# Kernel tuning notes

Hardware: AMD Instinct MI355X
Metric: run time of the kernel (lower is better)

Reference implementation:

```python
import jax, jax.numpy as jnp
import numpy as np

N = 50000      # nodes
E = 800000     # edges (avg degree 16)
F_IN = 128
HID = 128
C = 40
EPS = 1e-5     # BatchNorm1d eps


def setup_inputs() -> dict:
    key = jax.random.key(0)
    ks = jax.random.split(key, 8)

    def glorot(k, shape):
        lim = np.sqrt(6.0 / (shape[0] + shape[1])).astype(np.float32)
        return jax.random.uniform(k, shape, jnp.float32, -lim, lim)

    inp = {
        "features": jax.random.normal(ks[0], (N, F_IN), jnp.float32),
        "edge_index": jax.random.randint(ks[1], (2, E), 0, N, jnp.int32),
        "W1": glorot(ks[2], (F_IN, HID)), "b1": jnp.zeros((HID,), jnp.float32),
        "gamma1": jnp.ones((HID,), jnp.float32), "beta1": jnp.zeros((HID,), jnp.float32),
        "W2": glorot(ks[3], (HID, HID)), "b2": jnp.zeros((HID,), jnp.float32),
        "gamma2": jnp.ones((HID,), jnp.float32), "beta2": jnp.zeros((HID,), jnp.float32),
        "W3": glorot(ks[4], (HID, C)), "b3": jnp.zeros((C,), jnp.float32),
    }
    return inp


def _gcn_norm(edge_index):
    # Add self-loops and compute symmetric normalization D^-1/2 (A+I) D^-1/2
    loops = jnp.arange(N, dtype=edge_index.dtype)
    src = jnp.concatenate([edge_index[0], loops])
    dst = jnp.concatenate([edge_index[1], loops])
    deg = jax.ops.segment_sum(jnp.ones((E + N,), jnp.float32), dst, num_segments=N)
    dinv = jax.lax.rsqrt(jnp.maximum(deg, 1.0))
    return src, dst, dinv[src] * dinv[dst]  # per-edge norm coefficient


def _gcn_conv(x, W, b, src, dst, norm):
    h = x @ W                                   # [N, out]
    msg = h[src] * norm[:, None]                # gather + scale, [E+N, out]
    return jax.ops.segment_sum(msg, dst, num_segments=N) + b


def _bn(x, gamma, beta):
    # training-mode BatchNorm1d over the node axis (biased variance)
    mu = jnp.mean(x, axis=0)
    var = jnp.mean(jnp.square(x - mu), axis=0)
    return (x - mu) * jax.lax.rsqrt(var + EPS) * gamma + beta


def reference(features, edge_index, W1, b1, gamma1, beta1, W2, b2, gamma2, beta2, W3, b3):
    src, dst, norm = _gcn_norm(edge_index)
    h = jax.nn.relu(_bn(_gcn_conv(features, W1, b1, src, dst, norm), gamma1, beta1))
    h = jax.nn.relu(_bn(_gcn_conv(h, W2, b2, src, dst, norm), gamma2, beta2))
    h = _gcn_conv(h, W3, b3, src, dst, norm)
    return jax.nn.log_softmax(h, axis=-1)
```

## Files before the change

kernel.cpp:

```cpp
#include <hip/hip_runtime.h>
#include <math.h>

#define FEAT 128
#define NCLS 40
#define BN_EPS 1e-5f

typedef unsigned short u16;
typedef unsigned int u32;
typedef __attribute__((ext_vector_type(8))) short bf16x8;
typedef __attribute__((ext_vector_type(4))) float f32x4;

__device__ inline u32 f2b2(float a, float b) {
    u32 ua = __float_as_uint(a), ub = __float_as_uint(b);
    ua = (ua + 0x7fffu + ((ua >> 16) & 1u)) >> 16;
    ub = (ub + 0x7fffu + ((ub >> 16) & 1u)) >> 16;
    return ua | (ub << 16);
}
__device__ inline u16 f2b1(float a) {
    u32 ua = __float_as_uint(a);
    return (u16)((ua + 0x7fffu + ((ua >> 16) & 1u)) >> 16);
}
__device__ inline float b2f(u16 u) { return __uint_as_float((u32)u << 16); }
__device__ inline float4 b4fv(ushort4 u) {
    return make_float4(b2f(u.x), b2f(u.y), b2f(u.z), b2f(u.w));
}
__device__ inline float blo(u32 u) { return __uint_as_float(u << 16); }
__device__ inline float bhi(u32 u) { return __uint_as_float(u & 0xffff0000u); }

__device__ inline void b8acc(uint4 u, float w, float* a) {
    a[0] = fmaf(w, blo(u.x), a[0]); a[1] = fmaf(w, bhi(u.x), a[1]);
    a[2] = fmaf(w, blo(u.y), a[2]); a[3] = fmaf(w, bhi(u.y), a[3]);
    a[4] = fmaf(w, blo(u.z), a[4]); a[5] = fmaf(w, bhi(u.z), a[5]);
    a[6] = fmaf(w, blo(u.w), a[6]); a[7] = fmaf(w, bhi(u.w), a[7]);
}

#define WT_PITCH 136


__device__ inline void stage_wt(const float* __restrict__ W, u16* Wt) {
    const float4* W4 = (const float4*)W;
#pragma unroll
    for (int i = 0; i < 16; ++i) {
        int li = threadIdx.x + i * 256;
        int k = li >> 5;
        int n0 = (li & 31) * 4;
        float4 w = W4[li];
        Wt[(n0 + 0) * WT_PITCH + ((k + ((n0 + 0 & 3) << 5)) & 127)] = f2b1(w.x);
        Wt[(n0 + 1) * WT_PITCH + ((k + ((n0 + 1 & 3) << 5)) & 127)] = f2b1(w.y);
        Wt[(n0 + 2) * WT_PITCH + ((k + ((n0 + 2 & 3) << 5)) & 127)] = f2b1(w.z);
        Wt[(n0 + 3) * WT_PITCH + ((k + ((n0 + 3 & 3) << 5)) & 127)] = f2b1(w.w);
    }
}

__device__ inline void mfma_core(const u16* Wt, const bf16x8* bfrag,
                                 u16* __restrict__ Y, int node, int M, int nl, int quad) {
    f32x4 acc[8];
#pragma unroll
    for (int nt = 0; nt < 8; ++nt) acc[nt] = (f32x4){0.f, 0.f, 0.f, 0.f};
#pragma unroll
    for (int s = 0; s < 4; ++s) {
#pragma unroll
        for (int nt = 0; nt < 8; ++nt) {
            int nrow = nt * 16 + nl;
            int kk = ((s * 32 + quad * 8) + ((nl & 3) << 5)) & 127;
            uint4 aw = *(const uint4*)&Wt[nrow * WT_PITCH + kk];
            bf16x8 af = *(bf16x8*)&aw;
            acc[nt] = __builtin_amdgcn_mfma_f32_16x16x32_bf16(af, bfrag[s], acc[nt], 0, 0, 0);
        }
    }
    if (node < M) {
#pragma unroll
        for (int nt = 0; nt < 8; ++nt) {
            uint2 o;
            o.x = f2b2(acc[nt][0], acc[nt][1]);
            o.y = f2b2(acc[nt][2], acc[nt][3]);
            *(uint2*)&Y[(size_t)node * 128 + nt * 16 + quad * 4] = o;
        }
    }
}


__global__ __launch_bounds__(256) void k_l1_hist(
    const float* __restrict__ X, const float* __restrict__ W, u16* __restrict__ Y, int M,
    const int* __restrict__ dst, int* __restrict__ cnt, int E,
    int gemmBlocks, int histBlocks)
{
    __shared__ __align__(16) u16 Wt[128 * WT_PITCH];

    if ((int)blockIdx.x < gemmBlocks) {
        stage_wt(W, Wt);
        __syncthreads();

        int wv = threadIdx.x >> 6;
        int lane = threadIdx.x & 63;
        int nl = lane & 15, quad = lane >> 4;
        int node = blockIdx.x * 64 + wv * 16 + nl;

        bf16x8 bfrag[4];
        if (node < M) {
            const float4* xr = (const float4*)(X + (size_t)node * 128);
#pragma unroll
            for (int s = 0; s < 4; ++s) {
                float4 xa = xr[s * 8 + quad * 2];
                float4 xb = xr[s * 8 + quad * 2 + 1];
                uint4 bu;
                bu.x = f2b2(xa.x, xa.y); bu.y = f2b2(xa.z, xa.w);
                bu.z = f2b2(xb.x, xb.y); bu.w = f2b2(xb.z, xb.w);
                bfrag[s] = *(bf16x8*)&bu;
            }
        } else {
            uint4 z = make_uint4(0, 0, 0, 0);
#pragma unroll
            for (int s = 0; s < 4; ++s) bfrag[s] = *(bf16x8*)&z;
        }
        mfma_core(Wt, bfrag, Y, node, M, nl, quad);
    } else {
        int tb = blockIdx.x - gemmBlocks;
        int stride = histBlocks * 256;
        for (int e = tb * 256 + threadIdx.x; e < E; e += stride)
            atomicAdd(&cnt[dst[e]], 1);
    }
}


__global__ void k_scan_a(const int* __restrict__ cnt, int* __restrict__ bsum, int n) {
    int t = threadIdx.x;
    int idx = blockIdx.x * 512 + t * 2;
    int v = 0;
    if (idx < n) v += cnt[idx];
    if (idx + 1 < n) v += cnt[idx + 1];
    for (int d = 1; d < 64; d <<= 1) v += __shfl_xor(v, d, 64);
    __shared__ int ws[4];
    int lane = t & 63, w = t >> 6;
    if (lane == 0) ws[w] = v;
    __syncthreads();
    if (t == 0) bsum[blockIdx.x] = ws[0] + ws[1] + ws[2] + ws[3];
}

__global__ void k_scan_c(const int* __restrict__ cnt, const int* __restrict__ bsum,
                         int* __restrict__ row_off, int* __restrict__ cursor,
                         float* __restrict__ dinv, int n, int nb) {
    __shared__ int pre_s;
    __shared__ int wsum[4];
    int t = threadIdx.x;

    if (t < 128) {
        int v = (t < nb && t < (int)blockIdx.x) ? bsum[t] : 0;
        for (int d = 1; d < 64; d <<= 1) v += __shfl_xor(v, d, 64);
        __shared__ int halves[2];
        if ((t & 63) == 0) halves[t >> 6] = v;
        if (t == 0) {  }
        __syncthreads();
        if (t == 0) pre_s = halves[0] + halves[1];
    } else {
        __syncthreads();
    }
    __syncthreads();
    int pre = pre_s;

    int idx = blockIdx.x * 512 + t * 2;
    int v0 = (idx < n) ? cnt[idx] : 0;
    int v1 = (idx + 1 < n) ? cnt[idx + 1] : 0;
    int s = v0 + v1;
    int lane = t & 63, w = t >> 6;
    int incl = s;
    for (int d = 1; d < 64; d <<= 1) {
        int o = __shfl_up(incl, d, 64);
        if (lane >= d) incl += o;
    }
    if (lane == 63) wsum[w] = incl;
    __syncthreads();
    int wpre = 0;
    for (int i = 0; i < w; ++i) wpre += wsum[i];
    int base = pre + wpre + incl - s;
    if (idx < n) {
        row_off[idx] = base; cursor[idx] = base;
        dinv[idx] = rsqrtf((float)(v0 + 1));
    }
    if (idx + 1 < n) {
        row_off[idx + 1] = base + v0; cursor[idx + 1] = base + v0;
        dinv[idx + 1] = rsqrtf((float)(v1 + 1));
    }
    if ((int)blockIdx.x == nb - 1 && t == 0)
        row_off[n] = pre + wsum[0] + wsum[1] + wsum[2] + wsum[3];
}

__global__ __launch_bounds__(256) void k_fill(
    const int* __restrict__ src, const int* __restrict__ dst,
    int* __restrict__ cursor, int* __restrict__ col, float* __restrict__ wsrc,
    const float* __restrict__ dinv, int E, int n, int nchunks)
{
    int part = blockIdx.x & 7;
    int chunk = blockIdx.x >> 3;
    int lo = (int)(((long long)n * part) >> 3);
    int hi = (int)(((long long)n * (part + 1)) >> 3);
    int per = (E + nchunks - 1) / nchunks;
    int e0 = chunk * per;
    int e1 = e0 + per; if (e1 > E) e1 = E;
    for (int e = e0 + threadIdx.x; e < e1; e += 256) {
        int d = dst[e];
        if (d >= lo && d < hi) {
            int s = src[e];
            int p = atomicAdd(&cursor[d], 1);
            col[p] = s;
            wsrc[p] = dinv[s];
        }
    }
}


__global__ __launch_bounds__(256) void k_mfma_l2(
    const u16* __restrict__ X, const float* __restrict__ W,
    const float* __restrict__ sums, const float* __restrict__ gamma,
    const float* __restrict__ beta, u16* __restrict__ Y, int M)
{
    __shared__ __align__(16) u16 Wt[128 * WT_PITCH];
    __shared__ __align__(16) float scs[128], shs[128];

    if (threadIdx.x < 128) {
        int f = threadIdx.x;
        float inv_n = 1.f / (float)M;
        float mu = sums[f] * inv_n;
        float var = sums[128 + f] * inv_n - mu * mu;
        float rs = rsqrtf(var + BN_EPS);
        float sc = gamma[f] * rs;
        scs[f] = sc;
        shs[f] = beta[f] - mu * sc;
    }
    stage_wt(W, Wt);
    __syncthreads();

    int wv = threadIdx.x >> 6;
    int lane = threadIdx.x & 63;
    int nl = lane & 15, quad = lane >> 4;
    int node = blockIdx.x * 64 + wv * 16 + nl;

    bf16x8 bfrag[4];
    if (node < M) {
        const uint4* xr = (const uint4*)(X + (size_t)node * 128);
#pragma unroll
        for (int s = 0; s < 4; ++s) {
            int k0 = s * 32 + quad * 8;
            uint4 xu = xr[s * 4 + quad];
            float4 sc0 = *(const float4*)&scs[k0];
            float4 sc1 = *(const float4*)&scs[k0 + 4];
            float4 sh0 = *(const float4*)&shs[k0];
            float4 sh1 = *(const float4*)&shs[k0 + 4];
            float v0 = fmaxf(fmaf(blo(xu.x), sc0.x, sh0.x), 0.f);
            float v1 = fmaxf(fmaf(bhi(xu.x), sc0.y, sh0.y), 0.f);
            float v2 = fmaxf(fmaf(blo(xu.y), sc0.z, sh0.z), 0.f);
            float v3 = fmaxf(fmaf(bhi(xu.y), sc0.w, sh0.w), 0.f);
            float v4 = fmaxf(fmaf(blo(xu.z), sc1.x, sh1.x), 0.f);
            float v5 = fmaxf(fmaf(bhi(xu.z), sc1.y, sh1.y), 0.f);
            float v6 = fmaxf(fmaf(blo(xu.w), sc1.z, sh1.z), 0.f);
            float v7 = fmaxf(fmaf(bhi(xu.w), sc1.w, sh1.w), 0.f);
            uint4 bu;
            bu.x = f2b2(v0, v1); bu.y = f2b2(v2, v3);
            bu.z = f2b2(v4, v5); bu.w = f2b2(v6, v7);
            bfrag[s] = *(bf16x8*)&bu;
        }
    } else {
        uint4 z = make_uint4(0, 0, 0, 0);
#pragma unroll
        for (int s = 0; s < 4; ++s) bfrag[s] = *(bf16x8*)&z;
    }
    mfma_core(Wt, bfrag, Y, node, M, nl, quad);
}


__global__ __launch_bounds__(256) void k_gemm40(
    const u16* __restrict__ X, const float* __restrict__ W,
    const float* __restrict__ sums, const float* __restrict__ gamma,
    const float* __restrict__ beta, u16* __restrict__ Y, int M)
{
    __shared__ float Ws[128 * 40];
    __shared__ __align__(16) float scs[128], shs[128];
    __shared__ float Xs[32 * 260];

    int t = threadIdx.x;
    int row0 = blockIdx.x * 256;
    int tx = t & 3, ty = t >> 2;

    if (t < 128) {
        float inv_n = 1.f / (float)M;
        float mu = sums[t] * inv_n;
        float var = sums[128 + t] * inv_n - mu * mu;
        float rs = rsqrtf(var + BN_EPS);
        float sc = gamma[t] * rs;
        scs[t] = sc;
        shs[t] = beta[t] - mu * sc;
    }
    {
        const float4* W4 = (const float4*)W;
        float4* Ws4 = (float4*)Ws;
#pragma unroll
        for (int i = 0; i < 5; ++i) Ws4[t + i * 256] = W4[t + i * 256];
    }

    float acc[4][10];
#pragma unroll
    for (int r = 0; r < 4; ++r)
#pragma unroll
        for (int c = 0; c < 10; ++c) acc[r][c] = 0.f;

    for (int k0 = 0; k0 < 128; k0 += 32) {
        __syncthreads();
        {
            int rr = t >> 3;
            int kc = (t & 7) * 4;
            float4 sc = *(const float4*)&scs[k0 + kc];
            float4 sh = *(const float4*)&shs[k0 + kc];
#pragma unroll
            for (int p = 0; p < 8; ++p) {
                int r = rr + p * 32;
                int grow = row0 + r;
                float4 v = make_float4(0.f, 0.f, 0.f, 0.f);
                if (grow < M) v = b4fv(*(const ushort4*)(X + (size_t)grow * 128 + k0 + kc));
                v.x = fmaxf(fmaf(v.x, sc.x, sh.x), 0.f);
                v.y = fmaxf(fmaf(v.y, sc.y, sh.y), 0.f);
                v.z = fmaxf(fmaf(v.z, sc.z, sh.z), 0.f);
                v.w = fmaxf(fmaf(v.w, sc.w, sh.w), 0.f);
                Xs[(kc + 0) * 260 + r] = v.x;
                Xs[(kc + 1) * 260 + r] = v.y;
                Xs[(kc + 2) * 260 + r] = v.z;
                Xs[(kc + 3) * 260 + r] = v.w;
            }
        }
        __syncthreads();
#pragma unroll 8
        for (int kk = 0; kk < 32; ++kk) {
            const float4 xv = *(const float4*)&Xs[kk * 260 + ty * 4];
            const float xr[4] = {xv.x, xv.y, xv.z, xv.w};
            float wc[10];
#pragma unroll
            for (int c = 0; c < 5; ++c) {
                float2 w2 = *(const float2*)&Ws[(k0 + kk) * 40 + tx * 10 + c * 2];
                wc[c * 2] = w2.x; wc[c * 2 + 1] = w2.y;
            }
#pragma unroll
            for (int r = 0; r < 4; ++r)
#pragma unroll
                for (int c = 0; c < 10; ++c)
                    acc[r][c] = fmaf(xr[r], wc[c], acc[r][c]);
        }
    }

#pragma unroll
    for (int r = 0; r < 4; ++r) {
        int grow = row0 + ty * 4 + r;
        if (grow < M) {
            u32* yp = (u32*)(Y + (size_t)grow * 40 + tx * 10);
#pragma unroll
            for (int c = 0; c < 5; ++c)
                yp[c] = f2b2(acc[r][c * 2], acc[r][c * 2 + 1]);
        }
    }
}


__global__ __launch_bounds__(256) void k_agg128(
    const u16* __restrict__ t, const int* __restrict__ roff,
    const int* __restrict__ col, const float* __restrict__ wsrc,
    const float* __restrict__ dinv, const float* __restrict__ bias,
    u16* __restrict__ out, int n)
{
    int wid = threadIdx.x >> 4;
    int lane = threadIdx.x & 15;
    int i = blockIdx.x * 16 + wid;
    if (i >= n) return;
    int beg = roff[i], end = roff[i + 1];
    float di = dinv[i];

    float a[8];
    {
        uint4 su = ((const uint4*)(t + (size_t)i * 128))[lane];
        a[0] = di * blo(su.x); a[1] = di * bhi(su.x);
        a[2] = di * blo(su.y); a[3] = di * bhi(su.y);
        a[4] = di * blo(su.z); a[5] = di * bhi(su.z);
        a[6] = di * blo(su.w); a[7] = di * bhi(su.w);
    }

    int j = beg;
    for (; j + 7 < end; j += 8) {
        int s[8]; float w[8]; uint4 v[8];
#pragma unroll
        for (int k = 0; k < 8; ++k) { s[k] = col[j + k]; w[k] = wsrc[j + k]; }
#pragma unroll
        for (int k = 0; k < 8; ++k) v[k] = ((const uint4*)(t + (size_t)s[k] * 128))[lane];
#pragma unroll
        for (int k = 0; k < 8; ++k) b8acc(v[k], w[k], a);
    }
    for (; j < end; ++j) {
        float w0 = wsrc[j];
        uint4 v = ((const uint4*)(t + (size_t)col[j] * 128))[lane];
        b8acc(v, w0, a);
    }

    float4 bA = ((const float4*)bias)[lane * 2];
    float4 bB = ((const float4*)bias)[lane * 2 + 1];
    uint4 o;
    o.x = f2b2(fmaf(di, a[0], bA.x), fmaf(di, a[1], bA.y));
    o.y = f2b2(fmaf(di, a[2], bA.z), fmaf(di, a[3], bA.w));
    o.z = f2b2(fmaf(di, a[4], bB.x), fmaf(di, a[5], bB.y));
    o.w = f2b2(fmaf(di, a[6], bB.z), fmaf(di, a[7], bB.w));
    ((uint4*)(out + (size_t)i * 128))[lane] = o;
}


__global__ __launch_bounds__(256) void k_bnstats(const u16* __restrict__ a,
                                                 float* __restrict__ sums, int n) {
    int lane = threadIdx.x & 15;
    int rt = threadIdx.x >> 4;
    float s[8], q[8];
#pragma unroll
    for (int k = 0; k < 8; ++k) { s[k] = 0.f; q[k] = 0.f; }

    for (int i = blockIdx.x * 16 + rt; i < n; i += gridDim.x * 16) {
        uint4 u = ((const uint4*)(a + (size_t)i * 128))[lane];
        float v[8] = {blo(u.x), bhi(u.x), blo(u.y), bhi(u.y),
                      blo(u.z), bhi(u.z), blo(u.w), bhi(u.w)};
#pragma unroll
        for (int k = 0; k < 8; ++k) { s[k] += v[k]; q[k] = fmaf(v[k], v[k], q[k]); }
    }

    __shared__ float red[16][128];
#pragma unroll
    for (int k = 0; k < 8; ++k) red[rt][lane * 8 + k] = s[k];
    __syncthreads();
    if (threadIdx.x < 128) {
        float v = 0.f;
#pragma unroll
        for (int w = 0; w < 16; ++w) v += red[w][threadIdx.x];
        atomicAdd(&sums[threadIdx.x], v);
    }
    __syncthreads();
#pragma unroll
    for (int k = 0; k < 8; ++k) red[rt][lane * 8 + k] = q[k];
    __syncthreads();
    if (threadIdx.x < 128) {
        float v = 0.f;
#pragma unroll
        for (int w = 0; w < 16; ++w) v += red[w][threadIdx.x];
        atomicAdd(&sums[128 + threadIdx.x], v);
    }
}


__global__ __launch_bounds__(256) void k_agg40(
    const u16* __restrict__ t, const int* __restrict__ roff,
    const int* __restrict__ col, const float* __restrict__ wsrc,
    const float* __restrict__ dinv, const float* __restrict__ bias,
    float* __restrict__ out, int n)
{
    int i = blockIdx.x * 32 + (threadIdx.x >> 3);
    if (i >= n) return;
    int l = threadIdx.x & 7;
    bool act = l < 5;
    int beg = roff[i], end = roff[i + 1];
    float di = dinv[i];

    float a[8] = {0.f, 0.f, 0.f, 0.f, 0.f, 0.f, 0.f, 0.f};
    if (act) {
        uint4 su = ((const uint4*)(t + (size_t)i * NCLS))[l];
        a[0] = di * blo(su.x); a[1] = di * bhi(su.x);
        a[2] = di * blo(su.y); a[3] = di * bhi(su.y);
        a[4] = di * blo(su.z); a[5] = di * bhi(su.z);
        a[6] = di * blo(su.w); a[7] = di * bhi(su.w);
    }
    int j = beg;
    for (; j + 7 < end; j += 8) {
        int s[8]; float w[8]; uint4 v[8];
#pragma unroll
        for (int k = 0; k < 8; ++k) { s[k] = col[j + k]; w[k] = wsrc[j + k]; }
#pragma unroll
        for (int k = 0; k < 8; ++k)
            v[k] = act ? ((const uint4*)(t + (size_t)s[k] * NCLS))[l]
                       : make_uint4(0, 0, 0, 0);
#pragma unroll
        for (int k = 0; k < 8; ++k) b8acc(v[k], w[k], a);
    }
    for (; j < end; ++j) {
        float w0 = wsrc[j];
        uint4 v = act ? ((const uint4*)(t + (size_t)col[j] * NCLS))[l]
                      : make_uint4(0, 0, 0, 0);
        b8acc(v, w0, a);
    }

    float v[8];
    float m = -INFINITY;
    if (act) {
        float4 b0 = *(const float4*)(bias + l * 8);
        float4 b1 = *(const float4*)(bias + l * 8 + 4);
        v[0] = fmaf(di, a[0], b0.x); v[1] = fmaf(di, a[1], b0.y);
        v[2] = fmaf(di, a[2], b0.z); v[3] = fmaf(di, a[3], b0.w);
        v[4] = fmaf(di, a[4], b1.x); v[5] = fmaf(di, a[5], b1.y);
        v[6] = fmaf(di, a[6], b1.z); v[7] = fmaf(di, a[7], b1.w);
#pragma unroll
        for (int k = 0; k < 8; ++k) m = fmaxf(m, v[k]);
    }
#pragma unroll
    for (int d = 1; d < 8; d <<= 1) m = fmaxf(m, __shfl_xor(m, d, 8));
    float es = 0.f;
    if (act) {
#pragma unroll
        for (int k = 0; k < 8; ++k) es += expf(v[k] - m);
    }
#pragma unroll
    for (int d = 1; d < 8; d <<= 1) es += __shfl_xor(es, d, 8);
    float ls = logf(es);
    if (act) {
        float4 o0, o1;
        o0.x = v[0] - m - ls; o0.y = v[1] - m - ls;
        o0.z = v[2] - m - ls; o0.w = v[3] - m - ls;
        o1.x = v[4] - m - ls; o1.y = v[5] - m - ls;
        o1.z = v[6] - m - ls; o1.w = v[7] - m - ls;
        *(float4*)(out + (size_t)i * NCLS + l * 8) = o0;
        *(float4*)(out + (size_t)i * NCLS + l * 8 + 4) = o1;
    }
}


extern "C" void kernel_launch(void* const* d_in, const int* in_sizes, int n_in,
                              void* d_out, int out_size, void* d_ws, size_t ws_size,
                              hipStream_t stream) {
    const float* features = (const float*)d_in[0];
    const int* edge_index = (const int*)d_in[1];
    const float* W1 = (const float*)d_in[2];
    const float* b1 = (const float*)d_in[3];
    const float* gamma1 = (const float*)d_in[4];
    const float* beta1 = (const float*)d_in[5];
    const float* W2 = (const float*)d_in[6];
    const float* b2 = (const float*)d_in[7];
    const float* gamma2 = (const float*)d_in[8];
    const float* beta2 = (const float*)d_in[9];
    const float* W3 = (const float*)d_in[10];
    const float* b3 = (const float*)d_in[11];
    float* out = (float*)d_out;

    int n = in_sizes[0] / FEAT;
    int E = in_sizes[1] / 2;

    char* p = (char*)d_ws;
    auto alloc = [&](size_t bytes) -> void* {
        void* r = (void*)p;
        p += (bytes + 255) & ~(size_t)255;
        return r;
    };
    int* cnt     = (int*)alloc((size_t)n * 4);
    int* row_off = (int*)alloc((size_t)(n + 1) * 4);
    int* cursor  = (int*)alloc((size_t)n * 4);
    int* colb    = (int*)alloc((size_t)E * 4);
    float* wsrc  = (float*)alloc((size_t)E * 4);
    int* bsum    = (int*)alloc(1024);
    float* dinv  = (float*)alloc((size_t)n * 4);
    float* sums  = (float*)alloc(512 * 4);
    u16* hb      = (u16*)alloc((size_t)n * 128 * 2);
    u16* ab      = (u16*)alloc((size_t)n * 128 * 2);

    float* sums1 = sums;
    float* sums2 = sums + 256;

    const int* e_src = edge_index;
    const int* e_dst = edge_index + E;

    int gb64 = (n + 63) / 64;
    int gb16 = (n + 15) / 16;
    int gb32 = (n + 31) / 32;
    int nb = (n + 511) / 512;

    hipMemsetAsync(cnt, 0, (size_t)n * 4, stream);
    hipMemsetAsync(sums, 0, 512 * 4, stream);
    int histBlocks = 512;
    k_l1_hist<<<gb64 + histBlocks, 256, 0, stream>>>(features, W1, hb, n,
                                                     e_dst, cnt, E, gb64, histBlocks);
    k_scan_a<<<nb, 256, 0, stream>>>(cnt, bsum, n);
    k_scan_c<<<nb, 256, 0, stream>>>(cnt, bsum, row_off, cursor, dinv, n, nb);
    int nchunks = 160;
    k_fill<<<nchunks * 8, 256, 0, stream>>>(e_src, e_dst, cursor, colb, wsrc, dinv, E, n, nchunks);

    k_agg128<<<gb16, 256, 0, stream>>>(hb, row_off, colb, wsrc, dinv, b1, ab, n);
    k_bnstats<<<512, 256, 0, stream>>>(ab, sums1, n);

    k_mfma_l2<<<gb64, 256, 0, stream>>>(ab, W2, sums1, gamma1, beta1, hb, n);
    k_agg128<<<gb16, 256, 0, stream>>>(hb, row_off, colb, wsrc, dinv, b2, ab, n);
    k_bnstats<<<512, 256, 0, stream>>>(ab, sums2, n);

    k_gemm40<<<(n + 255) / 256, 256, 0, stream>>>(ab, W3, sums2, gamma2, beta2, hb, n);
    k_agg40<<<gb32, 256, 0, stream>>>(hb, row_off, colb, wsrc, dinv, b3, out, n);
}
```

Baseline: 350.1 us.

## Merge scan into single-block kernel, vectorize fill loads, coalesce memsets

Replaces the two-kernel block-sum/prefix scan with one 1024-thread single-block scan in which each thread serially walks a contiguous chunk of counts. This removes a launch and the cross-block dependency. Separately, the fill kernel now loads four destination indices at once with int4 and rounds each chunk up to a multiple of four, and the two memsets are merged into one by placing sums right after cnt. The risk is that the single block serially reads about 49 strided elements per thread, which coalesces poorly and could cost more than the saved launch.

```diff
diff --git a/kernel.cpp b/kernel.cpp
--- a/kernel.cpp
+++ b/kernel.cpp
@@ -123,66 +123,43 @@
 }
 
 
-__global__ void k_scan_a(const int* __restrict__ cnt, int* __restrict__ bsum, int n) {
+__global__ __launch_bounds__(1024) void k_scan(
+    const int* __restrict__ cnt, int* __restrict__ row_off, int* __restrict__ cursor,
+    float* __restrict__ dinv, int n)
+{
     int t = threadIdx.x;
-    int idx = blockIdx.x * 512 + t * 2;
-    int v = 0;
-    if (idx < n) v += cnt[idx];
-    if (idx + 1 < n) v += cnt[idx + 1];
-    for (int d = 1; d < 64; d <<= 1) v += __shfl_xor(v, d, 64);
-    __shared__ int ws[4];
-    int lane = t & 63, w = t >> 6;
-    if (lane == 0) ws[w] = v;
-    __syncthreads();
-    if (t == 0) bsum[blockIdx.x] = ws[0] + ws[1] + ws[2] + ws[3];
-}
-
-__global__ void k_scan_c(const int* __restrict__ cnt, const int* __restrict__ bsum,
-                         int* __restrict__ row_off, int* __restrict__ cursor,
-                         float* __restrict__ dinv, int n, int nb) {
-    __shared__ int pre_s;
-    __shared__ int wsum[4];
-    int t = threadIdx.x;
-
-    if (t < 128) {
-        int v = (t < nb && t < (int)blockIdx.x) ? bsum[t] : 0;
-        for (int d = 1; d < 64; d <<= 1) v += __shfl_xor(v, d, 64);
-        __shared__ int halves[2];
-        if ((t & 63) == 0) halves[t >> 6] = v;
-        if (t == 0) {  }
-        __syncthreads();
-        if (t == 0) pre_s = halves[0] + halves[1];
-    } else {
-        __syncthreads();
-    }
-    __syncthreads();
-    int pre = pre_s;
-
-    int idx = blockIdx.x * 512 + t * 2;
-    int v0 = (idx < n) ? cnt[idx] : 0;
-    int v1 = (idx + 1 < n) ? cnt[idx + 1] : 0;
-    int s = v0 + v1;
-    int lane = t & 63, w = t >> 6;
-    int incl = s;
+    int CH = (n + 1023) >> 10;
+    int s0 = t * CH;
+    int s1 = s0 + CH; if (s1 > n) s1 = n;
+
+    int sum = 0;
+    for (int i = s0; i < s1; ++i) sum += cnt[i];
+
+    int lane = t & 63, wv = t >> 6;
+    int incl = sum;
+#pragma unroll
     for (int d = 1; d < 64; d <<= 1) {
         int o = __shfl_up(incl, d, 64);
         if (lane >= d) incl += o;
     }
-    if (lane == 63) wsum[w] = incl;
+    __shared__ int wsum[16], woff[16];
+    if (lane == 63) wsum[wv] = incl;
     __syncthreads();
-    int wpre = 0;
-    for (int i = 0; i < w; ++i) wpre += wsum[i];
-    int base = pre + wpre + incl - s;
-    if (idx < n) {
-        row_off[idx] = base; cursor[idx] = base;
-        dinv[idx] = rsqrtf((float)(v0 + 1));
-    }
-    if (idx + 1 < n) {
-        row_off[idx + 1] = base + v0; cursor[idx + 1] = base + v0;
-        dinv[idx + 1] = rsqrtf((float)(v1 + 1));
-    }
-    if ((int)blockIdx.x == nb - 1 && t == 0)
-        row_off[n] = pre + wsum[0] + wsum[1] + wsum[2] + wsum[3];
+    if (t < 16) {
+        int v = 0;
+        for (int i = 0; i < t; ++i) v += wsum[i];
+        woff[t] = v;
+    }
+    __syncthreads();
+
+    int run = woff[wv] + incl - sum;
+    for (int i = s0; i < s1; ++i) {
+        int c = cnt[i];
+        row_off[i] = run; cursor[i] = run;
+        dinv[i] = rsqrtf((float)(c + 1));
+        run += c;
+    }
+    if (t == 1023) row_off[n] = run;
 }
 
 __global__ __launch_bounds__(256) void k_fill(
@@ -194,16 +171,34 @@
     int chunk = blockIdx.x >> 3;
     int lo = (int)(((long long)n * part) >> 3);
     int hi = (int)(((long long)n * (part + 1)) >> 3);
-    int per = (E + nchunks - 1) / nchunks;
+    int per = ((E + nchunks - 1) / nchunks + 3) & ~3;
     int e0 = chunk * per;
     int e1 = e0 + per; if (e1 > E) e1 = E;
-    for (int e = e0 + threadIdx.x; e < e1; e += 256) {
-        int d = dst[e];
-        if (d >= lo && d < hi) {
-            int s = src[e];
-            int p = atomicAdd(&cursor[d], 1);
-            col[p] = s;
-            wsrc[p] = dinv[s];
+
+    for (int eb = e0 + (int)threadIdx.x * 4; eb < e1; eb += 1024) {
+        if (eb + 4 <= e1) {
+            int4 d4 = *(const int4*)(dst + eb);
+            int dd[4] = {d4.x, d4.y, d4.z, d4.w};
+#pragma unroll
+            for (int k = 0; k < 4; ++k) {
+                int d = dd[k];
+                if (d >= lo && d < hi) {
+                    int s = src[eb + k];
+                    int p = atomicAdd(&cursor[d], 1);
+                    col[p] = s;
+                    wsrc[p] = dinv[s];
+                }
+            }
+        } else {
+            for (int e = eb; e < e1; ++e) {
+                int d = dst[e];
+                if (d >= lo && d < hi) {
+                    int s = src[e];
+                    int p = atomicAdd(&cursor[d], 1);
+                    col[p] = s;
+                    wsrc[p] = dinv[s];
+                }
+            }
         }
     }
 }
@@ -547,13 +542,13 @@
         return r;
     };
     int* cnt     = (int*)alloc((size_t)n * 4);
+    float* sums  = (float*)alloc(512 * 4);
+    size_t zspan = (size_t)((char*)(sums + 512) - (char*)cnt);
     int* row_off = (int*)alloc((size_t)(n + 1) * 4);
     int* cursor  = (int*)alloc((size_t)n * 4);
     int* colb    = (int*)alloc((size_t)E * 4);
     float* wsrc  = (float*)alloc((size_t)E * 4);
-    int* bsum    = (int*)alloc(1024);
     float* dinv  = (float*)alloc((size_t)n * 4);
-    float* sums  = (float*)alloc(512 * 4);
     u16* hb      = (u16*)alloc((size_t)n * 128 * 2);
     u16* ab      = (u16*)alloc((size_t)n * 128 * 2);
 
@@ -566,15 +561,12 @@
     int gb64 = (n + 63) / 64;
     int gb16 = (n + 15) / 16;
     int gb32 = (n + 31) / 32;
-    int nb = (n + 511) / 512;
-
-    hipMemsetAsync(cnt, 0, (size_t)n * 4, stream);
-    hipMemsetAsync(sums, 0, 512 * 4, stream);
+
+    hipMemsetAsync(cnt, 0, zspan, stream);
     int histBlocks = 512;
     k_l1_hist<<<gb64 + histBlocks, 256, 0, stream>>>(features, W1, hb, n,
                                                      e_dst, cnt, E, gb64, histBlocks);
-    k_scan_a<<<nb, 256, 0, stream>>>(cnt, bsum, n);
-    k_scan_c<<<nb, 256, 0, stream>>>(cnt, bsum, row_off, cursor, dinv, n, nb);
+    k_scan<<<1, 1024, 0, stream>>>(cnt, row_off, cursor, dinv, n);
     int nchunks = 160;
     k_fill<<<nchunks * 8, 256, 0, stream>>>(e_src, e_dst, cursor, colb, wsrc, dinv, E, n, nchunks);
 
```

Result: slower. 473.1 us (+35.1%).
